# Optimization experiments

Hardware: AMD Instinct MI355X
Metric: run time of the kernel (lower is better)

Reference implementation:

```python
import jax, jax.numpy as jnp
import numpy as np
from jax import lax

EPS = 1e-5

def conv2d(x, w, pad):
    return lax.conv_general_dilated(x, w, (1, 1), [(pad, pad), (pad, pad)],
                                    dimension_numbers=('NCHW', 'OIHW', 'NCHW'))

def bn(x, g, b, m, v):
    scale = (g / jnp.sqrt(v + EPS))[None, :, None, None]
    return (x - m[None, :, None, None]) * scale + b[None, :, None, None]

def upsample_bilinear_align_corners(x, scale):
    b, c, h, w = x.shape
    oh, ow = h * scale, w * scale
    ys = jnp.linspace(0.0, h - 1.0, oh)
    xs = jnp.linspace(0.0, w - 1.0, ow)
    y0 = jnp.floor(ys).astype(jnp.int32); y1 = jnp.minimum(y0 + 1, h - 1)
    x0 = jnp.floor(xs).astype(jnp.int32); x1 = jnp.minimum(x0 + 1, w - 1)
    wy = (ys - y0)[None, None, :, None]
    wx = (xs - x0)[None, None, None, :]
    rows = x[:, :, y0, :] * (1.0 - wy) + x[:, :, y1, :] * wy   # (b,c,oh,w)
    return rows[:, :, :, x0] * (1.0 - wx) + rows[:, :, :, x1] * wx

def setup_inputs() -> dict:
    key = jax.random.key(0)
    ks = jax.random.split(key, 12)
    Cin, C4, C8, NC = 2048, 512, 256, 19
    B, H, W = 4, 32, 32
    s = lambda fan: 1.0 / np.sqrt(fan)
    inp = {
        'x': jax.random.normal(ks[0], (B, Cin, H, W), dtype=jnp.float32),
        'conv1_w': jax.random.normal(ks[1], (C4, Cin, 3, 3), jnp.float32) * s(Cin * 9),
        'bn1_g': jnp.ones((C4,)), 'bn1_b': jnp.zeros((C4,)),
        'bn1_m': jnp.zeros((C4,)), 'bn1_v': jnp.ones((C4,)),
        'conv2_w': jax.random.normal(ks[2], (C4, Cin, 3, 3), jnp.float32) * s(Cin * 9),
        'bn2_g': jnp.ones((C4,)), 'bn2_b': jnp.zeros((C4,)),
        'bn2_m': jnp.zeros((C4,)), 'bn2_v': jnp.ones((C4,)),
        'pa_convB_w': jax.random.normal(ks[3], (C4, C4, 1, 1), jnp.float32) * s(C4),
        'pa_gamma': jnp.zeros((1,)),
        'ca_beta': jnp.zeros((1,)),
        'conv3_w': jax.random.normal(ks[4], (C4, C4, 3, 3), jnp.float32) * s(C4 * 9),
        'bn3_g': jnp.ones((C4,)), 'bn3_b': jnp.zeros((C4,)),
        'bn3_m': jnp.zeros((C4,)), 'bn3_v': jnp.ones((C4,)),
        'conv4a_w': jax.random.normal(ks[5], (C8, C4, 3, 3), jnp.float32) * s(C4 * 9),
        'bn4_g': jnp.ones((C8,)), 'bn4_b': jnp.zeros((C8,)),
        'bn4_m': jnp.zeros((C8,)), 'bn4_v': jnp.ones((C8,)),
        'conv4b_w': jax.random.normal(ks[6], (NC, C8, 3, 3), jnp.float32) * s(C8 * 9),
    }
    return inp

def position_attention(x, convB_w, gamma):
    b, c, h, w = x.shape
    # NOTE: original code uses convB for B, C and D (convC/convD unused) - faithful.
    Bm = conv2d(x, convB_w, 0).reshape(b, c, h * w)          # (b,c,hw)
    S = jax.nn.softmax(jnp.einsum('bcn,bcm->bnm', Bm, Bm), axis=-1)  # (b,hw,hw)
    E = jnp.einsum('bcm,bnm->bcn', Bm, S).reshape(b, c, h, w)
    return gamma * E + x

def channel_attention(x, beta):
    b, c, h, w = x.shape
    xf = x.reshape(b, c, h * w)
    A = jax.nn.softmax(jnp.einsum('bcn,bdn->bcd', xf, xf), axis=-1)  # (b,c,c)
    X = jnp.einsum('bkc,bkn->bcn', A, xf).reshape(b, c, h, w)        # A^T @ xf
    return beta * X + x

def reference(x, conv1_w, bn1_g, bn1_b, bn1_m, bn1_v,
              conv2_w, bn2_g, bn2_b, bn2_m, bn2_v,
              pa_convB_w, pa_gamma, ca_beta,
              conv3_w, bn3_g, bn3_b, bn3_m, bn3_v,
              conv4a_w, bn4_g, bn4_b, bn4_m, bn4_v, conv4b_w):
    x_pa = jax.nn.relu(bn(conv2d(x, conv1_w, 1), bn1_g, bn1_b, bn1_m, bn1_v))
    x_ca = jax.nn.relu(bn(conv2d(x, conv2_w, 1), bn2_g, bn2_b, bn2_m, bn2_v))
    pa = position_attention(x_pa, pa_convB_w, pa_gamma)
    ca = channel_attention(x_ca, ca_beta)
    out = jax.nn.relu(bn(conv2d(pa + ca, conv3_w, 1), bn3_g, bn3_b, bn3_m, bn3_v))
    out = upsample_bilinear_align_corners(out, 8)
    out = jax.nn.relu(bn(conv2d(out, conv4a_w, 1), bn4_g, bn4_b, bn4_m, bn4_v))
    out = conv2d(out, conv4b_w, 1)
    return out
```

## Files before the change

kernel.cpp:

```cpp
#include <hip/hip_runtime.h>
#include <stdint.h>

typedef __bf16 v8bf __attribute__((ext_vector_type(8)));
typedef float  v4f  __attribute__((ext_vector_type(4)));

#define MFMA16(a,b,c) __builtin_amdgcn_mfma_f32_16x16x32_bf16((a),(b),(c),0,0,0)

__device__ __forceinline__ void g2l16(void* lds, const void* g) {
  __builtin_amdgcn_global_load_lds(
      (__attribute__((address_space(1))) unsigned int*)g,
      (__attribute__((address_space(3))) unsigned int*)lds, 16, 0, 0);
}


__global__ void bnprep(const float* __restrict__ g, const float* __restrict__ b,
                       const float* __restrict__ m, const float* __restrict__ v,
                       float* __restrict__ sc, float* __restrict__ bi, int C) {
  int i = blockIdx.x * 256 + threadIdx.x;
  if (i < C) {
    float s = g[i] * rsqrtf(v[i] + 1e-5f);
    sc[i] = s;
    bi[i] = b[i] - m[i] * s;
  }
}

__global__ void pack_w(const float* __restrict__ src, __bf16* __restrict__ dst,
                       int co_cnt, int co_src, int co_off, int co_tot, int ci, int taps) {
  int idx = blockIdx.x * 256 + threadIdx.x;
  if (idx >= co_cnt * ci) return;
  int c = idx % ci, co = idx / ci;
  for (int t = 0; t < taps; ++t) {
    float v = (co < co_src) ? src[((size_t)co * ci + c) * taps + t] : 0.f;
    dst[((size_t)t * co_tot + co_off + co) * ci + c] = (__bf16)v;
  }
}

__global__ void cast_x_k(const float* __restrict__ x, __bf16* __restrict__ xb) {
  __shared__ float tl[64][65];
  int p0 = blockIdx.x * 64, c0 = blockIdx.y * 64, n = blockIdx.z;
  const float* xin = x + (size_t)n * 2048 * 1024;
  for (int it = 0; it < 16; ++it) {
    int idx = it * 256 + threadIdx.x;
    int px = idx & 63, cl = idx >> 6;
    tl[px][cl] = xin[(size_t)(c0 + cl) * 1024 + p0 + px];
  }
  __syncthreads();
  for (int it = 0; it < 16; ++it) {
    int idx = it * 256 + threadIdx.x;
    int cl = idx & 63, px = idx >> 6;
    xb[((size_t)n * 1024 + p0 + px) * 2048 + c0 + cl] = (__bf16)tl[px][cl];
  }
}

__global__ void trans_y2(const __bf16* __restrict__ y12, __bf16* __restrict__ y2t) {
  __shared__ __bf16 tl[64][72];
  int p0 = blockIdx.x * 64, c0 = blockIdx.y * 64, n = blockIdx.z;
  for (int it = 0; it < 16; ++it) {
    int idx = it * 256 + threadIdx.x;
    int cl = idx & 63, px = idx >> 6;
    tl[px][cl] = y12[((size_t)n * 1024 + p0 + px) * 1024 + 512 + c0 + cl];
  }
  __syncthreads();
  for (int it = 0; it < 16; ++it) {
    int idx = it * 256 + threadIdx.x;
    int px = idx & 63, cl = idx >> 6;
    y2t[((size_t)n * 512 + c0 + cl) * 1024 + p0 + px] = tl[px][cl];
  }
}

__global__ __launch_bounds__(256, 2)
void gemm_nt(const __bf16* __restrict__ A, const __bf16* __restrict__ B,
             size_t aB, size_t bB, int lda, int ldb, int kch, int mode,
             void* __restrict__ out, void* __restrict__ out2, size_t oB, int ldo) {
  __shared__ __align__(16) __bf16 tile[2][4 * 128 * 8];
  const int tid = threadIdx.x;
  const int lane = tid & 63, wv = tid >> 6;
  const int ln = lane & 15, q = lane >> 4;
  const int wm = wv >> 1, wn = wv & 1;
  const int p0 = blockIdx.x * 128, mb = blockIdx.y * 128, z = blockIdx.z;
  A += (size_t)z * aB; B += (size_t)z * bB;

  v4f acc[4][4];
#pragma unroll
  for (int mf = 0; mf < 4; ++mf)
#pragma unroll
    for (int nf = 0; nf < 4; ++nf)
#pragma unroll
      for (int r = 0; r < 4; ++r) acc[mf][nf][r] = 0.f;

  const __bf16* pa[4];
#pragma unroll
  for (int mf = 0; mf < 4; ++mf)
    pa[mf] = A + (size_t)(mb + wm * 64 + mf * 16 + ln) * lda + q * 8;

#pragma unroll
  for (int t2 = 0; t2 < 2; ++t2)
    g2l16(&tile[0][(wv * 128 + t2 * 64) * 8],
          B + (size_t)(p0 + t2 * 64 + lane) * ldb + wv * 8);
  __syncthreads();

  for (int kc = 0; kc < kch; ++kc) {
    const int tb = kc & 1;
    if (kc + 1 < kch) {
      const int c1 = (kc + 1) * 32;
#pragma unroll
      for (int t2 = 0; t2 < 2; ++t2)
        g2l16(&tile[tb ^ 1][(wv * 128 + t2 * 64) * 8],
              B + (size_t)(p0 + t2 * 64 + lane) * ldb + c1 + wv * 8);
    }
    const int c0 = kc * 32;
    v8bf bfr[4];
#pragma unroll
    for (int nf = 0; nf < 4; ++nf)
      bfr[nf] = *(const v8bf*)&tile[tb][(q * 128 + wn * 64 + nf * 16 + ln) * 8];
#pragma unroll
    for (int mf = 0; mf < 4; ++mf) {
      v8bf af = *(const v8bf*)(pa[mf] + c0);
#pragma unroll
      for (int nf = 0; nf < 4; ++nf)
        acc[mf][nf] = MFMA16(af, bfr[nf], acc[mf][nf]);
    }
    __syncthreads();
  }

#pragma unroll
  for (int mf = 0; mf < 4; ++mf) {
    const int m_l = wm * 64 + mf * 16 + q * 4;
#pragma unroll
    for (int nf = 0; nf < 4; ++nf) {
      const int n_l = wn * 64 + nf * 16 + ln;
      const int P = p0 + n_l;
      if (mode == 1) {
        float* o = (float*)out + (size_t)z * oB;
#pragma unroll
        for (int r = 0; r < 4; ++r)
          o[(size_t)(mb + m_l + r) * ldo + P] = acc[mf][nf][r];
      } else if (mode == 3) {
        float* o = (float*)out + (size_t)z * oB;
        v4f v;
#pragma unroll
        for (int r = 0; r < 4; ++r) v[r] = acc[mf][nf][r];
        *(v4f*)(o + (size_t)P * ldo + mb + m_l) = v;
      } else {
        __bf16* o = (__bf16*)out + (size_t)z * oB;
        union { __bf16 h[4]; uint2 u; } pk;
#pragma unroll
        for (int r = 0; r < 4; ++r) pk.h[r] = (__bf16)acc[mf][nf][r];
        *(uint2*)(o + (size_t)P * ldo + mb + m_l) = pk.u;
        if (mode == 2) {
          __bf16* o2 = (__bf16*)out2 + (size_t)z * oB;
#pragma unroll
          for (int r = 0; r < 4; ++r)
            o2[(size_t)(mb + m_l + r) * 1024 + P] = pk.h[r];
        }
      }
    }
  }
}

template <int CI, int KCH>
__global__ __launch_bounds__(256, 2)
void conv3x3_32(const __bf16* __restrict__ in, const __bf16* __restrict__ wp,
                const float* __restrict__ sc, const float* __restrict__ bi,
                __bf16* __restrict__ out, const int CO) {
  __shared__ __align__(16) __bf16 tile[2][816 * 8];
  __shared__ float s_sc[128], s_bi[128];
  const int tid = threadIdx.x;
  const int lane = tid & 63, wv = tid >> 6;
  const int ln = lane & 15, q = lane >> 4;
  const int pblk = blockIdx.x, cb = blockIdx.y;
  const int n = pblk >> 3, y0 = (pblk & 7) << 2;
  const int wm = wv >> 1, wn = wv & 1;

  if (tid < 128) { int c = cb * 128 + tid; s_sc[tid] = sc[c]; s_bi[tid] = bi[c]; }
  for (int t = tid; t < 1632; t += 256) ((uint4*)tile)[t] = make_uint4(0, 0, 0, 0);

  v4f acc[4][4];
#pragma unroll
  for (int mf = 0; mf < 4; ++mf)
#pragma unroll
    for (int nf = 0; nf < 4; ++nf)
#pragma unroll
      for (int r = 0; r < 4; ++r) acc[mf][nf][r] = 0.f;

  const __bf16* pa[4];
#pragma unroll
  for (int mf = 0; mf < 4; ++mf) {
    int co = cb * 128 + wm * 64 + mf * 16 + ln;
    pa[mf] = wp + (size_t)co * CI + q * 8;
  }
  int pixb[4];
#pragma unroll
  for (int nf = 0; nf < 4; ++nf) {
    int n_l = wn * 64 + nf * 16 + ln;
    pixb[nf] = (n_l >> 5) * 34 + (n_l & 31);
  }
  const __bf16* inb = in + (size_t)n * 1024 * CI;
  __syncthreads();

  if (lane < 32) {
#pragma unroll
    for (int t2 = 0; t2 < 6; ++t2) {
      int y = y0 - 1 + t2;
      if (y >= 0 && y < 32)
        g2l16(&tile[0][(wv * 204 + t2 * 34 + 1) * 8],
              inb + ((size_t)(y * 32 + lane) * CI + wv * 8));
    }
  }
  __syncthreads();

  for (int kc = 0; kc < KCH; ++kc) {
    const int tb = kc & 1;
    if (kc + 1 < KCH && lane < 32) {
      const int c1 = (kc + 1) * 32;
#pragma unroll
      for (int t2 = 0; t2 < 6; ++t2) {
        int y = y0 - 1 + t2;
        if (y >= 0 && y < 32)
          g2l16(&tile[tb ^ 1][(wv * 204 + t2 * 34 + 1) * 8],
                inb + ((size_t)(y * 32 + lane) * CI + c1 + wv * 8));
      }
    }
    const int ci0 = kc * 32;
#pragma unroll
    for (int tap = 0; tap < 9; ++tap) {
      const int ty = tap / 3, tx = tap % 3;
      v8bf bfr[4];
#pragma unroll
      for (int nf = 0; nf < 4; ++nf)
        bfr[nf] = *(const v8bf*)&tile[tb][(q * 204 + pixb[nf] + ty * 34 + tx) * 8];
      const size_t toff = (size_t)tap * CO * CI + ci0;
#pragma unroll
      for (int mf = 0; mf < 4; ++mf) {
        v8bf af = *(const v8bf*)(pa[mf] + toff);
#pragma unroll
        for (int nf = 0; nf < 4; ++nf)
          acc[mf][nf] = MFMA16(af, bfr[nf], acc[mf][nf]);
      }
    }
    __syncthreads();
  }

#pragma unroll
  for (int mf = 0; mf < 4; ++mf) {
    const int m_l = wm * 64 + mf * 16 + q * 4;
#pragma unroll
    for (int nf = 0; nf < 4; ++nf) {
      const int n_l = wn * 64 + nf * 16 + ln;
      const int p_img = (y0 + (n_l >> 5)) * 32 + (n_l & 31);
      union { __bf16 h[4]; uint2 u; } pk;
#pragma unroll
      for (int r = 0; r < 4; ++r) {
        float v = acc[mf][nf][r] * s_sc[m_l + r] + s_bi[m_l + r];
        pk.h[r] = (__bf16)fmaxf(v, 0.f);
      }
      *(uint2*)(out + (size_t)(n * 1024 + p_img) * CO + cb * 128 + m_l) = pk.u;
    }
  }
}

__global__ __launch_bounds__(256, 4)
void up_combine(const float* __restrict__ D, const float* __restrict__ sc,
                const float* __restrict__ bi, __bf16* __restrict__ y4) {
  const int tid = threadIdx.x;
  const int coq = blockIdx.x;
  const int oy = blockIdx.y;
  const int n = blockIdx.z;
  const int co = coq * 64 + (tid & 15) * 4;
  const int px0 = (tid >> 4) * 16;

  const v4f s4 = *(const v4f*)(sc + co);
  const v4f b4 = *(const v4f*)(bi + co);

  v4f acc[16];
#pragma unroll
  for (int j = 0; j < 16; ++j)
#pragma unroll
    for (int r = 0; r < 4; ++r) acc[j][r] = 0.f;

  const float* Dn = D + (size_t)n * 1024 * 2304;

#pragma unroll
  for (int ty = 0; ty < 3; ++ty) {
    int fy = oy + ty - 1;
    if (fy < 0 || fy > 255) continue;
    float syf = fy * (31.0f / 255.0f);
    int rA = (int)syf; float wy = syf - rA;
    int rB = rA < 31 ? rA + 1 : 31;
    float wA = 1.f - wy, wB = wy;
    const float* rowA = Dn + (size_t)rA * 32 * 2304;
    const float* rowB = Dn + (size_t)rB * 32 * 2304;
#pragma unroll
    for (int tx = 0; tx < 3; ++tx) {
      const int tco = (ty * 3 + tx) * 256 + co;
      int cur = -99;
      v4f a0{}, a1{}, b0{}, b1{};
#pragma unroll
      for (int j = 0; j < 16; ++j) {
        int fx = px0 + j + tx - 1;
        if (fx < 0 || fx > 255) continue;
        float sxf = fx * (31.0f / 255.0f);
        int c0 = (int)sxf; float wx = sxf - c0;
        if (c0 != cur) {
          cur = c0;
          int c1 = c0 < 31 ? c0 + 1 : 31;
          a0 = *(const v4f*)(rowA + (size_t)c0 * 2304 + tco);
          a1 = *(const v4f*)(rowA + (size_t)c1 * 2304 + tco);
          b0 = *(const v4f*)(rowB + (size_t)c0 * 2304 + tco);
          b1 = *(const v4f*)(rowB + (size_t)c1 * 2304 + tco);
        }
        float wxA = 1.f - wx;
        float cA = wA * wxA, cB = wA * wx, cC = wB * wxA, cD = wB * wx;
#pragma unroll
        for (int r = 0; r < 4; ++r)
          acc[j][r] += cA * a0[r] + cB * a1[r] + cC * b0[r] + cD * b1[r];
      }
    }
  }

  __bf16* ob = y4 + (((size_t)n * 65536 + (size_t)oy * 256 + px0) * 256 + co);
#pragma unroll
  for (int j = 0; j < 16; ++j) {
    union { __bf16 h[4]; uint2 u; } pk;
#pragma unroll
    for (int r = 0; r < 4; ++r) {
      float v = acc[j][r] * s4[r] + b4[r];
      pk.h[r] = (__bf16)fmaxf(v, 0.f);
    }
    *(uint2*)(ob + (size_t)j * 256) = pk.u;
  }
}

__global__ __launch_bounds__(256, 2)
void conv4b_k(const __bf16* __restrict__ y4, const __bf16* __restrict__ wp,
              float* __restrict__ outp) {
  __shared__ __align__(16) __bf16 tile[2][816 * 8];
  const int tid = threadIdx.x;
  const int lane = tid & 63, wv = tid >> 6;
  const int ln = lane & 15, q = lane >> 4;
  const int xblk = blockIdx.x, strip = blockIdx.y, n = blockIdx.z;
  const int oy0 = strip * 4, ox0 = xblk * 32;

  for (int t = tid; t < 1632; t += 256) ((uint4*)tile)[t] = make_uint4(0, 0, 0, 0);

  v4f acc[2][2];
#pragma unroll
  for (int mf = 0; mf < 2; ++mf)
#pragma unroll
    for (int nf = 0; nf < 2; ++nf)
#pragma unroll
      for (int r = 0; r < 4; ++r) acc[mf][nf][r] = 0.f;

  const __bf16* pa[2];
#pragma unroll
  for (int mf = 0; mf < 2; ++mf)
    pa[mf] = wp + (size_t)(mf * 16 + ln) * 256 + q * 8;
  int pixb[2];
#pragma unroll
  for (int nf = 0; nf < 2; ++nf) {
    int n_l = wv * 32 + nf * 16 + ln;
    pixb[nf] = (n_l >> 5) * 34 + (n_l & 31);
  }
  const __bf16* src = y4 + (size_t)n * 65536 * 256;
  const int gx = ox0 - 1 + lane;
  const bool xin = (lane < 34) && (gx >= 0) && (gx < 256);
  __syncthreads();

#pragma unroll
  for (int t2 = 0; t2 < 6; ++t2) {
    int y = oy0 - 1 + t2;
    if (y >= 0 && y < 256 && xin)
      g2l16(&tile[0][(wv * 204 + t2 * 34) * 8],
            src + ((size_t)(y * 256 + gx) * 256 + wv * 8));
  }
  __syncthreads();

  for (int kc = 0; kc < 8; ++kc) {
    const int tb = kc & 1;
    if (kc + 1 < 8) {
      const int c1 = (kc + 1) * 32;
#pragma unroll
      for (int t2 = 0; t2 < 6; ++t2) {
        int y = oy0 - 1 + t2;
        if (y >= 0 && y < 256 && xin)
          g2l16(&tile[tb ^ 1][(wv * 204 + t2 * 34) * 8],
                src + ((size_t)(y * 256 + gx) * 256 + c1 + wv * 8));
      }
    }
    const int ci0 = kc * 32;
#pragma unroll
    for (int tap = 0; tap < 9; ++tap) {
      const int ty = tap / 3, tx = tap % 3;
      v8bf bfr[2];
#pragma unroll
      for (int nf = 0; nf < 2; ++nf)
        bfr[nf] = *(const v8bf*)&tile[tb][(q * 204 + pixb[nf] + ty * 34 + tx) * 8];
      const size_t toff = (size_t)tap * 32 * 256 + ci0;
#pragma unroll
      for (int mf = 0; mf < 2; ++mf) {
        v8bf af = *(const v8bf*)(pa[mf] + toff);
#pragma unroll
        for (int nf = 0; nf < 2; ++nf)
          acc[mf][nf] = MFMA16(af, bfr[nf], acc[mf][nf]);
      }
    }
    __syncthreads();
  }

#pragma unroll
  for (int mf = 0; mf < 2; ++mf) {
    const int m_l = mf * 16 + q * 4;
#pragma unroll
    for (int nf = 0; nf < 2; ++nf) {
      const int n_l = wv * 32 + nf * 16 + ln;
      const int oy = oy0 + (n_l >> 5), ox = ox0 + (n_l & 31);
#pragma unroll
      for (int r = 0; r < 4; ++r) {
        int co = m_l + r;
        if (co < 19)
          outp[(((size_t)n * 19 + co) * 256 + oy) * 256 + ox] = acc[mf][nf][r];
      }
    }
  }
}


__global__ void softmax1024(const float* __restrict__ S, __bf16* __restrict__ O) {
  __shared__ float red[256];
  const int row = blockIdx.x, tid = threadIdx.x;
  const float* p = S + (size_t)row * 1024;
  float v0 = p[tid], v1 = p[tid + 256], v2 = p[tid + 512], v3 = p[tid + 768];
  float m = fmaxf(fmaxf(v0, v1), fmaxf(v2, v3));
  red[tid] = m; __syncthreads();
  for (int s = 128; s > 0; s >>= 1) { if (tid < s) red[tid] = fmaxf(red[tid], red[tid + s]); __syncthreads(); }
  m = red[0]; __syncthreads();
  v0 = __expf(v0 - m); v1 = __expf(v1 - m); v2 = __expf(v2 - m); v3 = __expf(v3 - m);
  red[tid] = v0 + v1 + v2 + v3; __syncthreads();
  for (int s = 128; s > 0; s >>= 1) { if (tid < s) red[tid] += red[tid + s]; __syncthreads(); }
  float inv = 1.0f / red[0];
  __bf16* o = O + (size_t)row * 1024;
  o[tid] = (__bf16)(v0 * inv); o[tid + 256] = (__bf16)(v1 * inv);
  o[tid + 512] = (__bf16)(v2 * inv); o[tid + 768] = (__bf16)(v3 * inv);
}

__global__ void softmaxT512(const float* __restrict__ S, __bf16* __restrict__ O) {
  __shared__ float red[256];
  const int row = blockIdx.x, tid = threadIdx.x;
  const float* p = S + (size_t)row * 512;
  float v0 = p[tid], v1 = p[tid + 256];
  float m = fmaxf(v0, v1);
  red[tid] = m; __syncthreads();
  for (int s = 128; s > 0; s >>= 1) { if (tid < s) red[tid] = fmaxf(red[tid], red[tid + s]); __syncthreads(); }
  m = red[0]; __syncthreads();
  v0 = __expf(v0 - m); v1 = __expf(v1 - m);
  red[tid] = v0 + v1; __syncthreads();
  for (int s = 128; s > 0; s >>= 1) { if (tid < s) red[tid] += red[tid + s]; __syncthreads(); }
  float inv = 1.0f / red[0];
  int n = row >> 9, c = row & 511;
  __bf16* o = O + (size_t)n * 262144 + c;
  o[(size_t)tid * 512] = (__bf16)(v0 * inv);
  o[(size_t)(tid + 256) * 512] = (__bf16)(v1 * inv);
}

__global__ void combine_z(const __bf16* __restrict__ y12, const __bf16* __restrict__ E,
                          const __bf16* __restrict__ X, const float* __restrict__ gp,
                          const float* __restrict__ bp, __bf16* __restrict__ z) {
  size_t i = (size_t)blockIdx.x * 256 + threadIdx.x;
  int pg = (int)(i >> 9), c = (int)(i & 511);
  float g = gp[0], b = bp[0];
  float v = (float)y12[(size_t)pg * 1024 + c] + (float)y12[(size_t)pg * 1024 + 512 + c] +
            g * (float)E[i] + b * (float)X[i];
  z[i] = (__bf16)v;
}


extern "C" void kernel_launch(void* const* d_in, const int* in_sizes, int n_in,
                              void* d_out, int out_size, void* d_ws, size_t ws_size,
                              hipStream_t stream) {
  const float* x    = (const float*)d_in[0];
  const float* w1   = (const float*)d_in[1];
  const float* bn1g = (const float*)d_in[2];
  const float* bn1b = (const float*)d_in[3];
  const float* bn1m = (const float*)d_in[4];
  const float* bn1v = (const float*)d_in[5];
  const float* w2   = (const float*)d_in[6];
  const float* bn2g = (const float*)d_in[7];
  const float* bn2b = (const float*)d_in[8];
  const float* bn2m = (const float*)d_in[9];
  const float* bn2v = (const float*)d_in[10];
  const float* wB   = (const float*)d_in[11];
  const float* gam  = (const float*)d_in[12];
  const float* bet  = (const float*)d_in[13];
  const float* w3   = (const float*)d_in[14];
  const float* bn3g = (const float*)d_in[15];
  const float* bn3b = (const float*)d_in[16];
  const float* bn3m = (const float*)d_in[17];
  const float* bn3v = (const float*)d_in[18];
  const float* w4a  = (const float*)d_in[19];
  const float* bn4g = (const float*)d_in[20];
  const float* bn4b = (const float*)d_in[21];
  const float* bn4m = (const float*)d_in[22];
  const float* bn4v = (const float*)d_in[23];
  const float* w4b  = (const float*)d_in[24];

  char* ws = (char*)d_ws;
  size_t off = 0;
  auto take = [&](size_t bytes) -> char* {
    char* p = ws + off;
    off += (bytes + 255) & ~(size_t)255;
    return p;
  };
  __bf16* w12b  = (__bf16*)take(9ULL * 1024 * 2048 * 2);
  __bf16* w3b   = (__bf16*)take(9ULL * 512 * 512 * 2);
  __bf16* w4ab  = (__bf16*)take(9ULL * 256 * 512 * 2);
  __bf16* w4bb  = (__bf16*)take(9ULL * 32 * 256 * 2);
  __bf16* wBb   = (__bf16*)take(512ULL * 512 * 2);
  float*  sc12  = (float*)take(1024 * 4);
  float*  bi12  = (float*)take(1024 * 4);
  float*  sc3   = (float*)take(512 * 4);
  float*  bi3   = (float*)take(512 * 4);
  float*  sc4   = (float*)take(256 * 4);
  float*  bi4   = (float*)take(256 * 4);
  __bf16* xb    = (__bf16*)take(4ULL * 1024 * 2048 * 2);
  __bf16* y12   = (__bf16*)take(4ULL * 1024 * 1024 * 2);
  __bf16* Bm_pc = (__bf16*)take(4ULL * 1024 * 512 * 2);
  __bf16* Bm_cp = (__bf16*)take(4ULL * 512 * 1024 * 2);
  float*  Smat  = (float*)take(4ULL * 1024 * 1024 * 4);
  __bf16* Ssm   = (__bf16*)take(4ULL * 1024 * 1024 * 2);
  __bf16* E_pc  = (__bf16*)take(4ULL * 1024 * 512 * 2);
  __bf16* y2t   = (__bf16*)take(4ULL * 512 * 1024 * 2);
  float*  Scc   = (float*)take(4ULL * 512 * 512 * 4);
  __bf16* AsmT  = (__bf16*)take(4ULL * 512 * 512 * 2);
  __bf16* X_pc  = (__bf16*)take(4ULL * 1024 * 512 * 2);
  __bf16* zb    = (__bf16*)take(4ULL * 1024 * 512 * 2);
  __bf16* y4    = (__bf16*)take(4ULL * 65536 * 256 * 2);
  __bf16* y3    = (__bf16*)take(4ULL * 1024 * 512 * 2);
  float* Dmat = (float*)xb;

  bnprep<<<2, 256, 0, stream>>>(bn1g, bn1b, bn1m, bn1v, sc12, bi12, 512);
  bnprep<<<2, 256, 0, stream>>>(bn2g, bn2b, bn2m, bn2v, sc12 + 512, bi12 + 512, 512);
  bnprep<<<2, 256, 0, stream>>>(bn3g, bn3b, bn3m, bn3v, sc3, bi3, 512);
  bnprep<<<1, 256, 0, stream>>>(bn4g, bn4b, bn4m, bn4v, sc4, bi4, 256);
  pack_w<<<4096, 256, 0, stream>>>(w1, w12b, 512, 512, 0, 1024, 2048, 9);
  pack_w<<<4096, 256, 0, stream>>>(w2, w12b, 512, 512, 512, 1024, 2048, 9);
  pack_w<<<1024, 256, 0, stream>>>(w3, w3b, 512, 512, 0, 512, 512, 9);
  pack_w<<<512, 256, 0, stream>>>(w4a, w4ab, 256, 256, 0, 256, 512, 9);
  pack_w<<<32, 256, 0, stream>>>(w4b, w4bb, 32, 19, 0, 32, 256, 9);
  pack_w<<<1024, 256, 0, stream>>>(wB, wBb, 512, 512, 0, 512, 512, 1);
  cast_x_k<<<dim3(16, 32, 4), 256, 0, stream>>>(x, xb);

  conv3x3_32<2048, 64><<<dim3(32, 8), 256, 0, stream>>>(xb, w12b, sc12, bi12, y12, 1024);

  gemm_nt<<<dim3(8, 4, 4), 256, 0, stream>>>(wBb, y12, 0, 1048576, 512, 1024, 16, 2,
                                             Bm_pc, Bm_cp, 524288, 512);
  gemm_nt<<<dim3(8, 8, 4), 256, 0, stream>>>(Bm_pc, Bm_pc, 524288, 524288, 512, 512, 16, 1,
                                             Smat, nullptr, 1048576, 1024);
  softmax1024<<<4096, 256, 0, stream>>>(Smat, Ssm);
  gemm_nt<<<dim3(8, 4, 4), 256, 0, stream>>>(Bm_cp, Ssm, 524288, 1048576, 1024, 1024, 32, 0,
                                             E_pc, nullptr, 524288, 512);

  trans_y2<<<dim3(16, 8, 4), 256, 0, stream>>>(y12, y2t);
  gemm_nt<<<dim3(4, 4, 4), 256, 0, stream>>>(y2t, y2t, 524288, 524288, 1024, 1024, 32, 1,
                                             Scc, nullptr, 262144, 512);
  softmaxT512<<<2048, 256, 0, stream>>>(Scc, AsmT);
  gemm_nt<<<dim3(8, 4, 4), 256, 0, stream>>>(AsmT, y12 + 512, 262144, 1048576, 512, 1024, 16, 0,
                                             X_pc, nullptr, 524288, 512);

  combine_z<<<8192, 256, 0, stream>>>(y12, E_pc, X_pc, gam, bet, zb);

  conv3x3_32<512, 16><<<dim3(32, 4), 256, 0, stream>>>(zb, w3b, sc3, bi3, y3, 512);

  gemm_nt<<<dim3(8, 18, 4), 256, 0, stream>>>(w4ab, y3, 0, 524288, 512, 512, 16, 3,
                                              Dmat, nullptr, 2359296, 2304);
  up_combine<<<dim3(4, 256, 4), 256, 0, stream>>>(Dmat, sc4, bi4, y4);

  conv4b_k<<<dim3(8, 64, 4), 256, 0, stream>>>(y4, w4bb, (float*)d_out);
}
```

Baseline: 1.307 ms.

## Split-K the 3x3 convolutions with a separate reduce+BN+ReLU kernel

The two 32x32 3x3 convolutions are split four ways along the input-channel dimension, so the grid grows from 256 (or 128) blocks to 1024 (or 512) and fills more of the GPU's compute units. Each split writes fp32 partial sums into a scratch buffer that reuses the y4 allocation. A new kernel then sums the partials and applies BN and ReLU. Launch bounds for these kernels and for conv4b are raised to allow more resident blocks, at the cost of extra global traffic for the fp32 partials and one more launch per convolution.

```diff
diff --git a/kernel.cpp b/kernel.cpp
--- a/kernel.cpp
+++ b/kernel.cpp
@@ -158,21 +158,20 @@
   }
 }
 
-template <int CI, int KCH>
-__global__ __launch_bounds__(256, 2)
-void conv3x3_32(const __bf16* __restrict__ in, const __bf16* __restrict__ wp,
-                const float* __restrict__ sc, const float* __restrict__ bi,
-                __bf16* __restrict__ out, const int CO) {
+template <int CI, int KCH, int KS>
+__global__ __launch_bounds__(256, 4)
+void conv3x3_sk(const __bf16* __restrict__ in, const __bf16* __restrict__ wp,
+                float* __restrict__ part, const int CO) {
   __shared__ __align__(16) __bf16 tile[2][816 * 8];
-  __shared__ float s_sc[128], s_bi[128];
   const int tid = threadIdx.x;
   const int lane = tid & 63, wv = tid >> 6;
   const int ln = lane & 15, q = lane >> 4;
-  const int pblk = blockIdx.x, cb = blockIdx.y;
+  const int pblk = blockIdx.x, cb = blockIdx.y, ks = blockIdx.z;
   const int n = pblk >> 3, y0 = (pblk & 7) << 2;
   const int wm = wv >> 1, wn = wv & 1;
-
-  if (tid < 128) { int c = cb * 128 + tid; s_sc[tid] = sc[c]; s_bi[tid] = bi[c]; }
+  const int KCN = KCH / KS;
+  const int kbase = ks * KCN;
+
   for (int t = tid; t < 1632; t += 256) ((uint4*)tile)[t] = make_uint4(0, 0, 0, 0);
 
   v4f acc[4][4];
@@ -187,7 +186,7 @@
 #pragma unroll
   for (int mf = 0; mf < 4; ++mf) {
     int co = cb * 128 + wm * 64 + mf * 16 + ln;
-    pa[mf] = wp + (size_t)co * CI + q * 8;
+    pa[mf] = wp + (size_t)co * CI + kbase * 32 + q * 8;
   }
   int pixb[4];
 #pragma unroll
@@ -195,7 +194,7 @@
     int n_l = wn * 64 + nf * 16 + ln;
     pixb[nf] = (n_l >> 5) * 34 + (n_l & 31);
   }
-  const __bf16* inb = in + (size_t)n * 1024 * CI;
+  const __bf16* inb = in + (size_t)n * 1024 * CI + kbase * 32;
   __syncthreads();
 
   if (lane < 32) {
@@ -209,9 +208,9 @@
   }
   __syncthreads();
 
-  for (int kc = 0; kc < KCH; ++kc) {
+  for (int kc = 0; kc < KCN; ++kc) {
     const int tb = kc & 1;
-    if (kc + 1 < KCH && lane < 32) {
+    if (kc + 1 < KCN && lane < 32) {
       const int c1 = (kc + 1) * 32;
 #pragma unroll
       for (int t2 = 0; t2 < 6; ++t2) {
@@ -241,6 +240,7 @@
     __syncthreads();
   }
 
+  float* po = part + ((size_t)ks * 4096 + (size_t)n * 1024) * CO;
 #pragma unroll
   for (int mf = 0; mf < 4; ++mf) {
     const int m_l = wm * 64 + mf * 16 + q * 4;
@@ -248,15 +248,34 @@
     for (int nf = 0; nf < 4; ++nf) {
       const int n_l = wn * 64 + nf * 16 + ln;
       const int p_img = (y0 + (n_l >> 5)) * 32 + (n_l & 31);
-      union { __bf16 h[4]; uint2 u; } pk;
-#pragma unroll
-      for (int r = 0; r < 4; ++r) {
-        float v = acc[mf][nf][r] * s_sc[m_l + r] + s_bi[m_l + r];
-        pk.h[r] = (__bf16)fmaxf(v, 0.f);
-      }
-      *(uint2*)(out + (size_t)(n * 1024 + p_img) * CO + cb * 128 + m_l) = pk.u;
-    }
-  }
+      *(v4f*)(po + (size_t)p_img * CO + cb * 128 + m_l) = acc[mf][nf];
+    }
+  }
+}
+
+template <int CO, int KS>
+__global__ __launch_bounds__(256, 8)
+void reduce_bn_relu(const float* __restrict__ part, const float* __restrict__ sc,
+                    const float* __restrict__ bi, __bf16* __restrict__ out) {
+  const size_t splitStride = (size_t)4096 * CO;
+  size_t gi = (size_t)blockIdx.x * 256 + threadIdx.x;
+  size_t row = gi / (CO / 4);
+  int c4 = (int)(gi % (CO / 4)) * 4;
+  const float* p = part + row * CO + c4;
+  v4f a = *(const v4f*)p;
+#pragma unroll
+  for (int s = 1; s < KS; ++s) {
+    v4f b = *(const v4f*)(p + s * splitStride);
+#pragma unroll
+    for (int r = 0; r < 4; ++r) a[r] += b[r];
+  }
+  const v4f s4 = *(const v4f*)(sc + c4);
+  const v4f b4 = *(const v4f*)(bi + c4);
+  union { __bf16 h[4]; uint2 u; } pk;
+#pragma unroll
+  for (int r = 0; r < 4; ++r)
+    pk.h[r] = (__bf16)fmaxf(a[r] * s4[r] + b4[r], 0.f);
+  *(uint2*)(out + row * CO + c4) = pk.u;
 }
 
 __global__ __launch_bounds__(256, 4)
@@ -331,7 +350,7 @@
   }
 }
 
-__global__ __launch_bounds__(256, 2)
+__global__ __launch_bounds__(256, 4)
 void conv4b_k(const __bf16* __restrict__ y4, const __bf16* __restrict__ wp,
               float* __restrict__ outp) {
   __shared__ __align__(16) __bf16 tile[2][816 * 8];
@@ -536,6 +555,7 @@
   __bf16* y4    = (__bf16*)take(4ULL * 65536 * 256 * 2);
   __bf16* y3    = (__bf16*)take(4ULL * 1024 * 512 * 2);
   float* Dmat = (float*)xb;
+  float* partK = (float*)y4;
 
   bnprep<<<2, 256, 0, stream>>>(bn1g, bn1b, bn1m, bn1v, sc12, bi12, 512);
   bnprep<<<2, 256, 0, stream>>>(bn2g, bn2b, bn2m, bn2v, sc12 + 512, bi12 + 512, 512);
@@ -549,7 +569,8 @@
   pack_w<<<1024, 256, 0, stream>>>(wB, wBb, 512, 512, 0, 512, 512, 1);
   cast_x_k<<<dim3(16, 32, 4), 256, 0, stream>>>(x, xb);
 
-  conv3x3_32<2048, 64><<<dim3(32, 8), 256, 0, stream>>>(xb, w12b, sc12, bi12, y12, 1024);
+  conv3x3_sk<2048, 64, 4><<<dim3(32, 8, 4), 256, 0, stream>>>(xb, w12b, partK, 1024);
+  reduce_bn_relu<1024, 4><<<4096, 256, 0, stream>>>(partK, sc12, bi12, y12);
 
   gemm_nt<<<dim3(8, 4, 4), 256, 0, stream>>>(wBb, y12, 0, 1048576, 512, 1024, 16, 2,
                                              Bm_pc, Bm_cp, 524288, 512);
@@ -568,7 +589,8 @@
 
   combine_z<<<8192, 256, 0, stream>>>(y12, E_pc, X_pc, gam, bet, zb);
 
-  conv3x3_32<512, 16><<<dim3(32, 4), 256, 0, stream>>>(zb, w3b, sc3, bi3, y3, 512);
+  conv3x3_sk<512, 16, 4><<<dim3(32, 4, 4), 256, 0, stream>>>(zb, w3b, partK, 512);
+  reduce_bn_relu<512, 4><<<2048, 256, 0, stream>>>(partK, sc3, bi3, y3);
 
   gemm_nt<<<dim3(8, 18, 4), 256, 0, stream>>>(w4ab, y3, 0, 524288, 512, 512, 16, 3,
                                               Dmat, nullptr, 2359296, 2304);
```

After: 1.301 ms. No clear change (-0.5%).
